# Kernel tuning notes

Hardware: AMD Instinct MI355X
Metric: run time of the kernel (lower is better)

Reference implementation:

```python
import jax, jax.numpy as jnp
import numpy as np

B, T, I, H, FF, C = 4096, 512, 13, 7, 512, 1


def setup_inputs() -> dict:
    key = jax.random.key(0)
    ks = jax.random.split(key, 9)
    s_ih = 1.0 / np.sqrt(H)
    return {
        "x": jax.random.normal(ks[0], (B, T, I), dtype=jnp.float32),
        # PyTorch LSTM params, gate order i,f,g,o, uniform(-1/sqrt(H), 1/sqrt(H))
        "w_ih": jax.random.uniform(ks[1], (4 * H, I), minval=-s_ih, maxval=s_ih, dtype=jnp.float32),
        "w_hh": jax.random.uniform(ks[2], (4 * H, H), minval=-s_ih, maxval=s_ih, dtype=jnp.float32),
        "b_ih": jax.random.uniform(ks[3], (4 * H,), minval=-s_ih, maxval=s_ih, dtype=jnp.float32),
        "b_hh": jax.random.uniform(ks[4], (4 * H,), minval=-s_ih, maxval=s_ih, dtype=jnp.float32),
        "fc1_w": jax.random.uniform(ks[5], (FF, H), minval=-s_ih, maxval=s_ih, dtype=jnp.float32),
        "fc1_b": jax.random.uniform(ks[6], (FF,), minval=-s_ih, maxval=s_ih, dtype=jnp.float32),
        "fc_w": jax.random.uniform(ks[7], (C, FF), minval=-1.0 / np.sqrt(FF), maxval=1.0 / np.sqrt(FF), dtype=jnp.float32),
        "fc_b": jax.random.uniform(ks[8], (C,), minval=-1.0 / np.sqrt(FF), maxval=1.0 / np.sqrt(FF), dtype=jnp.float32),
    }


def _lstm_last_hidden(x, w_ih, w_hh, b_ih, b_hh):
    # Precompute input contributions for all timesteps: [B, T, 4H]
    xg = jnp.einsum("bti,gi->btg", x, w_ih) + b_ih

    def step(carry, xg_t):
        h, c = carry
        gates = xg_t + h @ w_hh.T + b_hh  # [B, 4H]
        i, f, g, o = jnp.split(gates, 4, axis=-1)
        i = jax.nn.sigmoid(i)
        f = jax.nn.sigmoid(f)
        g = jnp.tanh(g)
        o = jax.nn.sigmoid(o)
        c = f * c + i * g
        h = o * jnp.tanh(c)
        return (h, c), None

    h0 = jnp.zeros((x.shape[0], w_hh.shape[1]), dtype=x.dtype)
    (hn, _), _ = jax.lax.scan(step, (h0, h0), jnp.swapaxes(xg, 0, 1))
    return hn  # [B, H]


def reference(x, w_ih, w_hh, b_ih, b_hh, fc1_w, fc1_b, fc_w, fc_b):
    # Dropout(0.1) is identity in eval mode.
    hn = _lstm_last_hidden(x, w_ih, w_hh, b_ih, b_hh)
    out = jax.nn.relu(hn)
    out = jax.nn.relu(out @ fc1_w.T + fc1_b)
    return out @ fc_w.T + fc_b  # [B, 1]
```

## Files before the change

kernel.cpp:

```cpp
#include <hip/hip_runtime.h>

#define BB 4096
#define TN 512
#define IN 13
#define HN 7
#define FFD 512
#define CT 16
#define NCK (TN / CT)
#define GPB 2

#if defined(__has_builtin)
#  if __has_builtin(__builtin_amdgcn_permlane16_swap)
#    define HAVE_PL16 1
#  endif
#endif

#define QB(v, q)    __int_as_float(__builtin_amdgcn_mov_dpp(__float_as_int(v), (q)*0x55, 0xF, 0xF, true))
#define RORF(v, n)  __int_as_float(__builtin_amdgcn_mov_dpp(__float_as_int(v), 0x120 + (n), 0xF, 0xF, true))

__device__ __forceinline__ void rowswap(float& a, float& b) {
#ifdef HAVE_PL16
    auto r = __builtin_amdgcn_permlane16_swap(__float_as_uint(a), __float_as_uint(b),
                                              false, false);
    a = __uint_as_float(r[0]);
    b = __uint_as_float(r[1]);
#else
    float ta, tb;
    asm volatile("v_mov_b32 %0, %2\n"
                 "v_mov_b32 %1, %3\n"
                 "s_nop 1\n"
                 "v_permlane16_swap_b32 %0, %1"
                 : "=&v"(ta), "=&v"(tb)
                 : "v"(a), "v"(b));
    a = ta; b = tb;
#endif
}

__device__ __forceinline__ float2 pkfma(float2 a, float2 b, float2 c) {
    float2 d;
    asm("v_pk_fma_f32 %0, %1, %2, %3" : "=v"(d) : "v"(a), "v"(b), "v"(c));
    return d;
}

__global__ __launch_bounds__(128, 4)
void lstm_fused(const float* __restrict__ x,
                const float* __restrict__ w_ih,
                const float* __restrict__ w_hh,
                const float* __restrict__ b_ih,
                const float* __restrict__ b_hh,
                const float* __restrict__ fc1_w,
                const float* __restrict__ fc1_b,
                const float* __restrict__ fc_w,
                const float* __restrict__ fc_b,
                float* __restrict__ out)
{
    __shared__ float2 xd2[2][CT/2][64];
    __shared__ float  xs[IN][GPB][CT];

    const int tid  = threadIdx.x;
    const int wid  = tid >> 6;
    const int l64  = tid & 63;
    const int grp  = l64 >> 5;
    const int lane = l64 & 31;
    const int b    = blockIdx.x * GPB + grp;

    const int tau = lane & 3;
    const int ju  = lane >> 2;
    const int jj  = (ju < HN) ? ju : (HN - 1);
    const int row = tau * HN + jj;
    const int jr  = ju & 3;

    const float L2E  = 1.4426950408889634f;
    const bool  is_tanh = (tau == 2);
    const float kmul = is_tanh ? (-2.0f * L2E) : (-L2E);
    const float sc   = is_tanh ?  2.0f : 1.0f;
    const float offc = is_tanh ? -1.0f : 0.0f;

    const int pr = __builtin_amdgcn_mov_dpp(l64, 0x124, 0xF, 0xF, true);
    const bool ror_plus = ((pr & 15) == ((l64 + 4) & 15));
    float paf = __int_as_float(l64);
    float pbf = __int_as_float(l64 + 64);
    rowswap(paf, pbf);
    const int pa = __float_as_int(paf) & 63;
    const bool a_even = (((pa >> 4) & 1) == 0);

    const int s_st = lane & 15;
    const int h_st = (lane >> 4) & 1;
    const int cb   = h_st * 7;
    float2 w2[IN];
    float2 bias2;
    float  p[7];

    float wA[4], wB[4];

    if (wid == 1) {
#pragma unroll
        for (int i = 0; i < IN; ++i) {
            const float w = kmul * w_ih[row * IN + i];
            w2[i] = make_float2(w, w);
        }
        const float bsum = kmul * (b_ih[row] + b_hh[row]);
        bias2 = make_float2(bsum, bsum);
    } else {
#pragma unroll
        for (int k = 0; k < 4; ++k) {
            const int dk  = ror_plus ? k : ((4 - k) & 3);
            const int cL  = (jr + dk) & 3;
            const int cH  = 4 + ((jr + dk) & 3);
            const float wL = kmul * w_hh[row * HN + cL];
            const float wH = (cH < HN) ? kmul * w_hh[row * HN + cH] : 0.0f;
            wA[k] = a_even ? wL : wH;
            wB[k] = a_even ? wH : wL;
        }
    }

    float a0 = 0.f, a1 = 0.f, a2 = 0.f, a3 = 0.f;
    float b0 = 0.f, b1 = 0.f, b2 = 0.f, b3 = 0.f;
    float cval = 0.0f;
    float hq_final = 0.0f;

    if (wid == 1) {
        const float* src0 = x + ((long)b * TN + s_st) * IN + cb;
#pragma unroll
        for (int c = 0; c < 6; ++c) p[c] = src0[c];
        if (h_st == 0) p[6] = src0[6];
#pragma unroll
        for (int c = 0; c < 6; ++c) xs[cb + c][grp][s_st] = p[c];
        if (h_st == 0) xs[cb + 6][grp][s_st] = p[6];
        {
            const float* src1 = x + ((long)b * TN + CT + s_st) * IN + cb;
#pragma unroll
            for (int c = 0; c < 6; ++c) p[c] = src1[c];
            if (h_st == 0) p[6] = src1[6];
        }
#pragma unroll
        for (int q = 0; q < CT; q += 4) {
            float2 accA = bias2, accB = bias2;
#pragma unroll
            for (int i = 0; i < IN; ++i) {
                const float4 xv = *(const float4*)&xs[i][grp][q];
                accA = pkfma(w2[i], make_float2(xv.x, xv.y), accA);
                accB = pkfma(w2[i], make_float2(xv.z, xv.w), accB);
            }
            xd2[0][(q >> 1) + 0][l64] = accA;
            xd2[0][(q >> 1) + 1][l64] = accB;
        }
    }
    __syncthreads();

    for (int ck = 0; ck < NCK; ++ck) {
        if (wid == 1) {
            const int nk = ck + 1;
            if (nk < NCK) {
#pragma unroll
                for (int c = 0; c < 6; ++c) xs[cb + c][grp][s_st] = p[c];
                if (h_st == 0) xs[cb + 6][grp][s_st] = p[6];
                if (nk + 1 < NCK) {
                    const float* src = x + ((long)b * TN + (nk + 1) * CT + s_st) * IN + cb;
#pragma unroll
                    for (int c = 0; c < 6; ++c) p[c] = src[c];
                    if (h_st == 0) p[6] = src[6];
                }
                const int buf = nk & 1;
#pragma unroll
                for (int q = 0; q < CT; q += 4) {
                    float2 accA = bias2, accB = bias2;
#pragma unroll
                    for (int i = 0; i < IN; ++i) {
                        const float4 xv = *(const float4*)&xs[i][grp][q];
                        accA = pkfma(w2[i], make_float2(xv.x, xv.y), accA);
                        accB = pkfma(w2[i], make_float2(xv.z, xv.w), accB);
                    }
                    xd2[buf][(q >> 1) + 0][l64] = accA;
                    xd2[buf][(q >> 1) + 1][l64] = accB;
                }
            }
        } else {
            const int buf = ck & 1;
            float xr[CT];
#pragma unroll
            for (int pq = 0; pq < CT / 2; ++pq) {
                const float2 v = xd2[buf][pq][l64];
                xr[2 * pq]     = v.x;
                xr[2 * pq + 1] = v.y;
            }
#pragma unroll
            for (int s = 0; s < CT; ++s) {
                float t0 = fmaf(wA[0], a0, xr[s]);
                t0 = fmaf(wA[1], a1, t0);
                t0 = fmaf(wA[2], a2, t0);
                t0 = fmaf(wA[3], a3, t0);
                float t1 = wB[0] * b0;
                t1 = fmaf(wB[1], b1, t1);
                t1 = fmaf(wB[2], b2, t1);
                t1 = fmaf(wB[3], b3, t1);
                const float sg = t0 + t1;

                float e   = __builtin_amdgcn_exp2f(sg);
                float val = fmaf(__builtin_amdgcn_rcpf(1.0f + e), sc, offc);

                const float iv = QB(val, 0);
                const float fv = QB(val, 1);
                const float gv = QB(val, 2);
                const float ov = QB(val, 3);

                cval = fmaf(fv, cval, iv * gv);
                float e2 = __builtin_amdgcn_exp2f(-2.0f * L2E * cval);
                float th = fmaf(__builtin_amdgcn_rcpf(1.0f + e2), 2.0f, -1.0f);
                const float hq = ov * th;
                hq_final = hq;

                a0 = hq; b0 = hq;
                rowswap(a0, b0);
                a1 = RORF(a0, 4);
                a2 = RORF(a0, 8);
                a3 = RORF(a0, 12);
                b1 = RORF(b0, 4);
                b2 = RORF(b0, 8);
                b3 = RORF(b0, 12);
            }
        }
        __syncthreads();
    }

    if (wid == 1) return;

    float hb[HN];
#pragma unroll
    for (int j = 0; j < HN; ++j) hb[j] = fmaxf(__shfl(hq_final, 4 * j, 32), 0.0f);

    float acc = 0.0f;
#pragma unroll
    for (int k = 0; k < FFD / 32; ++k) {
        const int r = lane + (k << 5);
        float s = fc1_b[r];
#pragma unroll
        for (int j = 0; j < HN; ++j) s = fmaf(fc1_w[r * HN + j], hb[j], s);
        s = fmaxf(s, 0.0f);
        acc = fmaf(fc_w[r], s, acc);
    }
#pragma unroll
    for (int o = 16; o >= 1; o >>= 1) acc += __shfl_xor(acc, o, 32);
    if (lane == 0) out[b] = acc + fc_b[0];
}

extern "C" void kernel_launch(void* const* d_in, const int* in_sizes, int n_in,
                              void* d_out, int out_size, void* d_ws, size_t ws_size,
                              hipStream_t stream) {
    const float* x     = (const float*)d_in[0];
    const float* w_ih  = (const float*)d_in[1];
    const float* w_hh  = (const float*)d_in[2];
    const float* b_ih  = (const float*)d_in[3];
    const float* b_hh  = (const float*)d_in[4];
    const float* fc1_w = (const float*)d_in[5];
    const float* fc1_b = (const float*)d_in[6];
    const float* fc_w  = (const float*)d_in[7];
    const float* fc_b  = (const float*)d_in[8];
    float* out = (float*)d_out;

    dim3 grid(BB / GPB);
    dim3 block(128);
    hipLaunchKernelGGL(lstm_fused, grid, block, 0, stream,
                       x, w_ih, w_hh, b_ih, b_hh, fc1_w, fc1_b, fc_w, fc_b, out);
}
```

Measured before the change: 110.7 us.

## Double chunk length and use lane-per-timestep loads with raw barrier handoff

Doubles the timestep chunk from 16 to 32, which halves the number of producer/consumer barrier handoffs across the sequence. Each producer lane now loads one full 13-float timestep row instead of the earlier split half-row scheme. The __syncthreads is replaced by an explicit lgkmcnt wait plus s_barrier wrapped in sched_barriers, so the compiler cannot move code across it. The cost is more registers for the larger xr buffer and larger LDS buffers, and the consumer has to wait longer before the first chunk is ready.

```diff
diff --git a/kernel.cpp b/kernel.cpp
--- a/kernel.cpp
+++ b/kernel.cpp
@@ -5,7 +5,7 @@
 #define IN 13
 #define HN 7
 #define FFD 512
-#define CT 16
+#define CT 32
 #define NCK (TN / CT)
 #define GPB 2
 
@@ -84,12 +84,10 @@
     const int pa = __float_as_int(paf) & 63;
     const bool a_even = (((pa >> 4) & 1) == 0);
 
-    const int s_st = lane & 15;
-    const int h_st = (lane >> 4) & 1;
-    const int cb   = h_st * 7;
     float2 w2[IN];
     float2 bias2;
-    float  p[7];
+    float  p[IN];
+    const float* xbase = x + (long)b * TN * IN;
 
     float wA[4], wB[4];
 
@@ -119,74 +117,64 @@
     float cval = 0.0f;
     float hq_final = 0.0f;
 
+#define LOADP(ck) do {                                                        \
+        const float* _s = xbase + (long)((ck) * CT + lane) * IN;              \
+        _Pragma("unroll")                                                     \
+        for (int _i = 0; _i < IN; ++_i) p[_i] = _s[_i];                       \
+    } while (0)
+#define COMMITP() do {                                                        \
+        _Pragma("unroll")                                                     \
+        for (int _i = 0; _i < IN; ++_i) xs[_i][grp][lane] = p[_i];            \
+    } while (0)
+#define PROJECT(ck) do {                                                      \
+        const int _buf = (ck) & 1;                                            \
+        _Pragma("unroll")                                                     \
+        for (int _q = 0; _q < CT; _q += 4) {                                  \
+            float2 _aA = bias2, _aB = bias2;                                  \
+            _Pragma("unroll")                                                 \
+            for (int _i = 0; _i < IN; ++_i) {                                 \
+                const float4 _xv = *(const float4*)&xs[_i][grp][_q];          \
+                _aA = pkfma(w2[_i], make_float2(_xv.x, _xv.y), _aA);          \
+                _aB = pkfma(w2[_i], make_float2(_xv.z, _xv.w), _aB);          \
+            }                                                                 \
+            xd2[_buf][(_q >> 1) + 0][l64] = _aA;                              \
+            xd2[_buf][(_q >> 1) + 1][l64] = _aB;                              \
+        }                                                                     \
+    } while (0)
+
+#define HANDOFF() do {                                                        \
+        if (wid == 1) { asm volatile("s_waitcnt lgkmcnt(0)" ::: "memory"); }  \
+        __builtin_amdgcn_sched_barrier(0);                                    \
+        __builtin_amdgcn_s_barrier();                                         \
+        __builtin_amdgcn_sched_barrier(0);                                    \
+    } while (0)
+
     if (wid == 1) {
-        const float* src0 = x + ((long)b * TN + s_st) * IN + cb;
-#pragma unroll
-        for (int c = 0; c < 6; ++c) p[c] = src0[c];
-        if (h_st == 0) p[6] = src0[6];
-#pragma unroll
-        for (int c = 0; c < 6; ++c) xs[cb + c][grp][s_st] = p[c];
-        if (h_st == 0) xs[cb + 6][grp][s_st] = p[6];
-        {
-            const float* src1 = x + ((long)b * TN + CT + s_st) * IN + cb;
-#pragma unroll
-            for (int c = 0; c < 6; ++c) p[c] = src1[c];
-            if (h_st == 0) p[6] = src1[6];
-        }
-#pragma unroll
-        for (int q = 0; q < CT; q += 4) {
-            float2 accA = bias2, accB = bias2;
-#pragma unroll
-            for (int i = 0; i < IN; ++i) {
-                const float4 xv = *(const float4*)&xs[i][grp][q];
-                accA = pkfma(w2[i], make_float2(xv.x, xv.y), accA);
-                accB = pkfma(w2[i], make_float2(xv.z, xv.w), accB);
-            }
-            xd2[0][(q >> 1) + 0][l64] = accA;
-            xd2[0][(q >> 1) + 1][l64] = accB;
-        }
-    }
-    __syncthreads();
+        LOADP(0);
+        COMMITP();
+        LOADP(1);
+        PROJECT(0);
+    }
+    HANDOFF();
 
     for (int ck = 0; ck < NCK; ++ck) {
         if (wid == 1) {
             const int nk = ck + 1;
             if (nk < NCK) {
-#pragma unroll
-                for (int c = 0; c < 6; ++c) xs[cb + c][grp][s_st] = p[c];
-                if (h_st == 0) xs[cb + 6][grp][s_st] = p[6];
-                if (nk + 1 < NCK) {
-                    const float* src = x + ((long)b * TN + (nk + 1) * CT + s_st) * IN + cb;
-#pragma unroll
-                    for (int c = 0; c < 6; ++c) p[c] = src[c];
-                    if (h_st == 0) p[6] = src[6];
-                }
-                const int buf = nk & 1;
-#pragma unroll
-                for (int q = 0; q < CT; q += 4) {
-                    float2 accA = bias2, accB = bias2;
-#pragma unroll
-                    for (int i = 0; i < IN; ++i) {
-                        const float4 xv = *(const float4*)&xs[i][grp][q];
-                        accA = pkfma(w2[i], make_float2(xv.x, xv.y), accA);
-                        accB = pkfma(w2[i], make_float2(xv.z, xv.w), accB);
-                    }
-                    xd2[buf][(q >> 1) + 0][l64] = accA;
-                    xd2[buf][(q >> 1) + 1][l64] = accB;
-                }
+                COMMITP();
+                if (nk + 1 < NCK) LOADP(nk + 1);
+                PROJECT(nk);
             }
         } else {
             const int buf = ck & 1;
-            float xr[CT];
-#pragma unroll
-            for (int pq = 0; pq < CT / 2; ++pq) {
-                const float2 v = xd2[buf][pq][l64];
-                xr[2 * pq]     = v.x;
-                xr[2 * pq + 1] = v.y;
-            }
+            float2 xr2[CT / 2];
+#pragma unroll
+            for (int pq = 0; pq < CT / 2; ++pq) xr2[pq] = xd2[buf][pq][l64];
+
 #pragma unroll
             for (int s = 0; s < CT; ++s) {
-                float t0 = fmaf(wA[0], a0, xr[s]);
+                const float xr = (s & 1) ? xr2[s >> 1].y : xr2[s >> 1].x;
+                float t0 = fmaf(wA[0], a0, xr);
                 t0 = fmaf(wA[1], a1, t0);
                 t0 = fmaf(wA[2], a2, t0);
                 t0 = fmaf(wA[3], a3, t0);
@@ -220,7 +208,7 @@
                 b3 = RORF(b0, 12);
             }
         }
-        __syncthreads();
+        HANDOFF();
     }
 
     if (wid == 1) return;
```

After: 100.9 us. -8.9%, faster.
